# Kernel optimization log

Hardware: AMD Instinct MI355X
Metric: run time of the kernel (lower is better)

The kernel has to match this reference:

```python
import jax, jax.numpy as jnp
import numpy as np
from jax import lax

C_IN, C_OUT, K, N_BASE, HIDDEN = 256, 256, 3, 8, 128
ATT_TAU = 1.0


def setup_inputs() -> dict:
    key = jax.random.key(0)
    ks = jax.random.split(key, 6)
    B, H, W = 64, 64, 64
    x = jax.random.normal(ks[0], (B, C_IN, H, W), dtype=jnp.float32)
    # attention MLP params (torch Linear convention: W is [out, in])
    w1 = jax.random.normal(ks[1], (HIDDEN, C_IN), dtype=jnp.float32) * (1.0 / np.sqrt(C_IN))
    b1 = jnp.zeros((HIDDEN,), dtype=jnp.float32)
    w2 = jax.random.normal(ks[2], (C_OUT * N_BASE, HIDDEN), dtype=jnp.float32) * (1.0 / np.sqrt(HIDDEN))
    b2 = jnp.zeros((C_OUT * N_BASE,), dtype=jnp.float32)
    # base filters: kaiming-normal over flat [n_base, c_in*k*k]
    fan_in = C_IN * K * K
    base_filters = jax.random.normal(ks[3], (N_BASE, fan_in), dtype=jnp.float32) * np.sqrt(2.0 / fan_in)
    return {"x": x, "w1": w1, "b1": b1, "w2": w2, "b2": b2, "base_filters": base_filters}


def reference(x, w1, b1, w2, b2, base_filters):
    B = x.shape[0]
    # global average pool -> [B, c_in]
    pooled = x.mean(axis=(2, 3))
    # attention MLP -> per-sample mixing weights [B, c_out, n_base]
    h = jax.nn.relu(pooled @ w1.T + b1)
    mix = (h @ w2.T + b2).reshape(B, C_OUT, N_BASE)
    mix = jax.nn.softmax(mix / ATT_TAU, axis=2)
    # base conv: [B, c_in, H, W] -> [B, n_base, H, W], SAME padding (k//2)
    filt = base_filters.reshape(N_BASE, C_IN, K, K)
    pad = K // 2
    y = lax.conv_general_dilated(
        x, filt, window_strides=(1, 1), padding=[(pad, pad), (pad, pad)],
        dimension_numbers=("NCHW", "OIHW", "NCHW"))
    # per-sample 1x1 mixing conv == batched matmul over channels
    out = jnp.einsum("bon,bnhw->bohw", mix, y)
    return out
```

## Files before the change

### kernel.cpp

```cpp
#include <hip/hip_runtime.h>
#include <math.h>

#define CIN 256
#define COUT 256
#define NB 8
#define HID 128
#define HW 4096
#define BATCH 64

__global__ __launch_bounds__(256) void repack_filters(
    const float* __restrict__ bf, float* __restrict__ fT) {
  int i = blockIdx.x * 256 + threadIdx.x;
  if (i < 8 * 2304) {
    int n = i / 2304;
    int cd = i % 2304;
    fT[cd * 8 + n] = bf[i];
  }
}

__global__ __launch_bounds__(256) void conv_pool_kernel(
    const float* __restrict__ x, const float* __restrict__ fT,
    float* __restrict__ ypart, float* __restrict__ poolpart) {
  __shared__ float xs[8 * 34 * 68];
  const int t = threadIdx.x;
  const int bid = blockIdx.x;
  const int b = bid >> 2;
  const int chhalf = (bid >> 1) & 1;
  const int rchunk = bid & 1;
  const int row0 = rchunk * 32;
  const int c0 = chhalf * 128;

  for (int i = t; i < 8 * 34 * 68; i += 256) xs[i] = 0.0f;
  __syncthreads();

  const int ch = t >> 5;
  const int part = t & 31;
  const int r = t >> 3;
  const int cg = t & 7;

  float acc[8][8];
#pragma unroll
  for (int n = 0; n < 8; ++n)
#pragma unroll
    for (int j = 0; j < 8; ++j) acc[n][j] = 0.0f;

  for (int chunk = 0; chunk < 16; ++chunk) {
    const int cbase = c0 + chunk * 8;
    float psum = 0.0f;
    const float* xsrc = x + ((size_t)(b * CIN + cbase + ch) * HW);
#pragma unroll
    for (int i = 0; i < 17; ++i) {
      int s = part + i * 32;
      int row = s >> 4;
      int seg = s & 15;
      int grow = row0 + row - 1;
      if (grow >= 0 && grow < 64) {
        const float4 v = *(const float4*)(xsrc + grow * 64 + seg * 4);
        float* dst = &xs[(ch * 34 + row) * 68 + 1 + seg * 4];
        dst[0] = v.x; dst[1] = v.y; dst[2] = v.z; dst[3] = v.w;
        if (row >= 1 && row < 33) psum += (v.x + v.y) + (v.z + v.w);
      }
    }
#pragma unroll
    for (int off = 16; off > 0; off >>= 1)
      psum += __shfl_down(psum, off, 32);
    if (part == 0)
      poolpart[(b * 2 + rchunk) * 256 + cbase + ch] = psum;
    __syncthreads();

#pragma unroll
    for (int cc = 0; cc < 8; ++cc) {
      const float* fb = fT + (size_t)(cbase + cc) * 72;
      const float* xrow = &xs[(cc * 34 + r) * 68 + cg * 8];
#pragma unroll
      for (int dy = 0; dy < 3; ++dy) {
        const float* xr = xrow + dy * 68;
        float w[10];
        float4 a0 = *(const float4*)(xr);
        float4 a1 = *(const float4*)(xr + 4);
        float2 a2 = *(const float2*)(xr + 8);
        w[0] = a0.x; w[1] = a0.y; w[2] = a0.z; w[3] = a0.w;
        w[4] = a1.x; w[5] = a1.y; w[6] = a1.z; w[7] = a1.w;
        w[8] = a2.x; w[9] = a2.y;
#pragma unroll
        for (int dx = 0; dx < 3; ++dx) {
#pragma unroll
          for (int n = 0; n < 8; ++n) {
            const float fv = fb[(dy * 3 + dx) * 8 + n];
#pragma unroll
            for (int j = 0; j < 8; ++j)
              acc[n][j] = fmaf(w[j + dx], fv, acc[n][j]);
          }
        }
      }
    }
    __syncthreads();
  }

#pragma unroll
  for (int n = 0; n < 8; ++n) {
    float* yp = ypart +
        ((size_t)(((b * 2 + chhalf) * 8 + n) * 64 + row0 + r) * 64 + cg * 8);
    float4 v0 = {acc[n][0], acc[n][1], acc[n][2], acc[n][3]};
    float4 v1 = {acc[n][4], acc[n][5], acc[n][6], acc[n][7]};
    *(float4*)(yp) = v0;
    *(float4*)(yp + 4) = v1;
  }
}

__global__ __launch_bounds__(256) void mlp_kernel(
    const float* __restrict__ poolpart, const float* __restrict__ w1,
    const float* __restrict__ b1, const float* __restrict__ w2,
    const float* __restrict__ b2, float* __restrict__ mix) {
  __shared__ float pool_s[256];
  __shared__ float h_s[128];
  const int t = threadIdx.x;
  const int b = blockIdx.x;
  pool_s[t] = (poolpart[(b * 2 + 0) * 256 + t] +
               poolpart[(b * 2 + 1) * 256 + t]) * (1.0f / 4096.0f);
  __syncthreads();
  if (t < 128) {
    float a = b1[t];
    const float* wr = w1 + t * 256;
    for (int c = 0; c < 256; c += 4) {
      float4 wv = *(const float4*)(wr + c);
      a = fmaf(pool_s[c], wv.x, a);
      a = fmaf(pool_s[c + 1], wv.y, a);
      a = fmaf(pool_s[c + 2], wv.z, a);
      a = fmaf(pool_s[c + 3], wv.w, a);
    }
    h_s[t] = fmaxf(a, 0.0f);
  }
  __syncthreads();
  float m[8];
#pragma unroll
  for (int n = 0; n < 8; ++n) {
    float a = b2[t * 8 + n];
    const float* wr = w2 + (size_t)(t * 8 + n) * 128;
    for (int j = 0; j < 128; j += 4) {
      float4 wv = *(const float4*)(wr + j);
      a = fmaf(h_s[j], wv.x, a);
      a = fmaf(h_s[j + 1], wv.y, a);
      a = fmaf(h_s[j + 2], wv.z, a);
      a = fmaf(h_s[j + 3], wv.w, a);
    }
    m[n] = a;
  }
  float mx = m[0];
#pragma unroll
  for (int n = 1; n < 8; ++n) mx = fmaxf(mx, m[n]);
  float s = 0.0f;
#pragma unroll
  for (int n = 0; n < 8; ++n) {
    m[n] = __expf(m[n] - mx);
    s += m[n];
  }
  float inv = 1.0f / s;
#pragma unroll
  for (int n = 0; n < 8; ++n) mix[(size_t)(b * 256 + t) * 8 + n] = m[n] * inv;
}

__global__ __launch_bounds__(256) void mix_conv_kernel(
    const float* __restrict__ ypart, const float* __restrict__ mix,
    float* __restrict__ out) {
  __shared__ float ys[8 * 1024];
  __shared__ float mix_s[2048];
  const int t = threadIdx.x;
  const int b = blockIdx.x >> 2;
  const int tile = blockIdx.x & 3;
  const int p0 = tile * 1024;

  const float* y0 = ypart + (size_t)(b * 2 + 0) * 8 * HW + p0;
  const float* y1 = ypart + (size_t)(b * 2 + 1) * 8 * HW + p0;
  for (int i = t; i < 2048; i += 256) {
    int n = i >> 8;
    int pv = i & 255;
    float4 a = *(const float4*)(y0 + n * HW + pv * 4);
    float4 c = *(const float4*)(y1 + n * HW + pv * 4);
    float4 r = {a.x + c.x, a.y + c.y, a.z + c.z, a.w + c.w};
    *(float4*)&ys[n * 1024 + pv * 4] = r;
  }
  {
    const float4* ms = (const float4*)(mix + (size_t)b * 2048);
    float4* md = (float4*)mix_s;
    for (int i = t; i < 512; i += 256) md[i] = ms[i];
  }
  __syncthreads();

  float4 y4[8];
#pragma unroll
  for (int n = 0; n < 8; ++n) y4[n] = *(const float4*)&ys[n * 1024 + t * 4];

  float* op = out + (size_t)b * COUT * HW + p0 + t * 4;
  for (int o = 0; o < 256; ++o) {
    float4 ma = *(const float4*)&mix_s[o * 8];
    float4 mb = *(const float4*)&mix_s[o * 8 + 4];
    float4 r;
    r.x = ma.x * y4[0].x; r.y = ma.x * y4[0].y;
    r.z = ma.x * y4[0].z; r.w = ma.x * y4[0].w;
    r.x = fmaf(ma.y, y4[1].x, r.x); r.y = fmaf(ma.y, y4[1].y, r.y);
    r.z = fmaf(ma.y, y4[1].z, r.z); r.w = fmaf(ma.y, y4[1].w, r.w);
    r.x = fmaf(ma.z, y4[2].x, r.x); r.y = fmaf(ma.z, y4[2].y, r.y);
    r.z = fmaf(ma.z, y4[2].z, r.z); r.w = fmaf(ma.z, y4[2].w, r.w);
    r.x = fmaf(ma.w, y4[3].x, r.x); r.y = fmaf(ma.w, y4[3].y, r.y);
    r.z = fmaf(ma.w, y4[3].z, r.z); r.w = fmaf(ma.w, y4[3].w, r.w);
    r.x = fmaf(mb.x, y4[4].x, r.x); r.y = fmaf(mb.x, y4[4].y, r.y);
    r.z = fmaf(mb.x, y4[4].z, r.z); r.w = fmaf(mb.x, y4[4].w, r.w);
    r.x = fmaf(mb.y, y4[5].x, r.x); r.y = fmaf(mb.y, y4[5].y, r.y);
    r.z = fmaf(mb.y, y4[5].z, r.z); r.w = fmaf(mb.y, y4[5].w, r.w);
    r.x = fmaf(mb.z, y4[6].x, r.x); r.y = fmaf(mb.z, y4[6].y, r.y);
    r.z = fmaf(mb.z, y4[6].z, r.z); r.w = fmaf(mb.z, y4[6].w, r.w);
    r.x = fmaf(mb.w, y4[7].x, r.x); r.y = fmaf(mb.w, y4[7].y, r.y);
    r.z = fmaf(mb.w, y4[7].z, r.z); r.w = fmaf(mb.w, y4[7].w, r.w);
    *(float4*)(op + (size_t)o * HW) = r;
  }
}

extern "C" void kernel_launch(void* const* d_in, const int* in_sizes, int n_in,
                              void* d_out, int out_size, void* d_ws,
                              size_t ws_size, hipStream_t stream) {
  const float* x  = (const float*)d_in[0];
  const float* w1 = (const float*)d_in[1];
  const float* b1 = (const float*)d_in[2];
  const float* w2 = (const float*)d_in[3];
  const float* b2 = (const float*)d_in[4];
  const float* bf = (const float*)d_in[5];
  float* out = (float*)d_out;

  char* ws = (char*)d_ws;
  float* ypart    = (float*)(ws);
  float* poolpart = (float*)(ws + 16777216);
  float* mixw     = (float*)(ws + 16777216 + 131072);
  float* fT       = (float*)(ws + 16777216 + 131072 + 2097152);

  repack_filters<<<72, 256, 0, stream>>>(bf, fT);
  conv_pool_kernel<<<256, 256, 0, stream>>>(x, fT, ypart, poolpart);
  mlp_kernel<<<64, 256, 0, stream>>>(poolpart, w1, b1, w2, b2, mixw);
  mix_conv_kernel<<<256, 256, 0, stream>>>(ypart, mixw, out);
}
```

Measured before the change: 692.3 us.

## Split conv into smaller tiles and channel quarters for more blocks

New measurement: 581.1 us. 16.1% less time.

```diff
diff --git a/kernel.cpp b/kernel.cpp
--- a/kernel.cpp
+++ b/kernel.cpp
@@ -7,6 +7,9 @@
 #define HID 128
 #define HW 4096
 #define BATCH 64
+
+#define TROWS 18
+#define XSTR 68
 
 __global__ __launch_bounds__(256) void repack_filters(
     const float* __restrict__ bf, float* __restrict__ fT) {
@@ -18,77 +21,76 @@
   }
 }
 
-__global__ __launch_bounds__(256) void conv_pool_kernel(
+__global__ __launch_bounds__(256, 4) void conv_pool_kernel(
     const float* __restrict__ x, const float* __restrict__ fT,
     float* __restrict__ ypart, float* __restrict__ poolpart) {
-  __shared__ float xs[8 * 34 * 68];
+  __shared__ float xs[8 * TROWS * XSTR];
   const int t = threadIdx.x;
   const int bid = blockIdx.x;
-  const int b = bid >> 2;
-  const int chhalf = (bid >> 1) & 1;
-  const int rchunk = bid & 1;
-  const int row0 = rchunk * 32;
-  const int c0 = chhalf * 128;
-
-  for (int i = t; i < 8 * 34 * 68; i += 256) xs[i] = 0.0f;
+  const int b = bid >> 4;
+  const int g = (bid >> 2) & 3;
+  const int rc = bid & 3;
+  const int row0 = rc * 16;
+  const int c0 = g * 64;
+
+  for (int i = t; i < 8 * TROWS * XSTR; i += 256) xs[i] = 0.0f;
   __syncthreads();
 
   const int ch = t >> 5;
   const int part = t & 31;
-  const int r = t >> 3;
-  const int cg = t & 7;
-
-  float acc[8][8];
+  const int r = t >> 4;
+  const int cg = t & 15;
+
+  float acc[8][4];
 #pragma unroll
   for (int n = 0; n < 8; ++n)
 #pragma unroll
-    for (int j = 0; j < 8; ++j) acc[n][j] = 0.0f;
-
-  for (int chunk = 0; chunk < 16; ++chunk) {
+    for (int j = 0; j < 4; ++j) acc[n][j] = 0.0f;
+
+#pragma unroll 1
+  for (int chunk = 0; chunk < 8; ++chunk) {
     const int cbase = c0 + chunk * 8;
     float psum = 0.0f;
     const float* xsrc = x + ((size_t)(b * CIN + cbase + ch) * HW);
 #pragma unroll
-    for (int i = 0; i < 17; ++i) {
+    for (int i = 0; i < 9; ++i) {
       int s = part + i * 32;
       int row = s >> 4;
       int seg = s & 15;
       int grow = row0 + row - 1;
       if (grow >= 0 && grow < 64) {
         const float4 v = *(const float4*)(xsrc + grow * 64 + seg * 4);
-        float* dst = &xs[(ch * 34 + row) * 68 + 1 + seg * 4];
+        float* dst = &xs[(ch * TROWS + row) * XSTR + 1 + seg * 4];
         dst[0] = v.x; dst[1] = v.y; dst[2] = v.z; dst[3] = v.w;
-        if (row >= 1 && row < 33) psum += (v.x + v.y) + (v.z + v.w);
+        if (row >= 1 && row <= 16) psum += (v.x + v.y) + (v.z + v.w);
       }
     }
 #pragma unroll
     for (int off = 16; off > 0; off >>= 1)
       psum += __shfl_down(psum, off, 32);
     if (part == 0)
-      poolpart[(b * 2 + rchunk) * 256 + cbase + ch] = psum;
+      poolpart[(b * 4 + rc) * 256 + cbase + ch] = psum;
     __syncthreads();
 
 #pragma unroll
     for (int cc = 0; cc < 8; ++cc) {
       const float* fb = fT + (size_t)(cbase + cc) * 72;
-      const float* xrow = &xs[(cc * 34 + r) * 68 + cg * 8];
+      const float* xrow = &xs[(cc * TROWS + r) * XSTR + cg * 4];
 #pragma unroll
       for (int dy = 0; dy < 3; ++dy) {
-        const float* xr = xrow + dy * 68;
-        float w[10];
+        const float* xr = xrow + dy * XSTR;
         float4 a0 = *(const float4*)(xr);
-        float4 a1 = *(const float4*)(xr + 4);
-        float2 a2 = *(const float2*)(xr + 8);
+        float2 a1 = *(const float2*)(xr + 4);
+        float w[6];
         w[0] = a0.x; w[1] = a0.y; w[2] = a0.z; w[3] = a0.w;
-        w[4] = a1.x; w[5] = a1.y; w[6] = a1.z; w[7] = a1.w;
-        w[8] = a2.x; w[9] = a2.y;
+        w[4] = a1.x; w[5] = a1.y;
 #pragma unroll
         for (int dx = 0; dx < 3; ++dx) {
 #pragma unroll
           for (int n = 0; n < 8; ++n) {
             const float fv = fb[(dy * 3 + dx) * 8 + n];
 #pragma unroll
-            for (int j = 0; j < 8; ++j)
+            for (int j = 0; j < 4; ++j)
               acc[n][j] = fmaf(w[j + dx], fv, acc[n][j]);
           }
         }
@@ -100,11 +102,9 @@
 #pragma unroll
   for (int n = 0; n < 8; ++n) {
     float* yp = ypart +
-        ((size_t)(((b * 2 + chhalf) * 8 + n) * 64 + row0 + r) * 64 + cg * 8);
+        ((size_t)(((b * 4 + g) * 8 + n) * 64 + row0 + r) * 64 + cg * 4);
     float4 v0 = {acc[n][0], acc[n][1], acc[n][2], acc[n][3]};
-    float4 v1 = {acc[n][4], acc[n][5], acc[n][6], acc[n][7]};
     *(float4*)(yp) = v0;
-    *(float4*)(yp + 4) = v1;
   }
 }
 
@@ -116,8 +116,10 @@
   __shared__ float h_s[128];
   const int t = threadIdx.x;
   const int b = blockIdx.x;
-  pool_s[t] = (poolpart[(b * 2 + 0) * 256 + t] +
-               poolpart[(b * 2 + 1) * 256 + t]) * (1.0f / 4096.0f);
+  pool_s[t] = (poolpart[(b * 4 + 0) * 256 + t] +
+               poolpart[(b * 4 + 1) * 256 + t] +
+               poolpart[(b * 4 + 2) * 256 + t] +
+               poolpart[(b * 4 + 3) * 256 + t]) * (1.0f / 4096.0f);
   __syncthreads();
   if (t < 128) {
     float a = b1[t];
@@ -170,15 +172,18 @@
   const int tile = blockIdx.x & 3;
   const int p0 = tile * 1024;
 
-  const float* y0 = ypart + (size_t)(b * 2 + 0) * 8 * HW + p0;
-  const float* y1 = ypart + (size_t)(b * 2 + 1) * 8 * HW + p0;
+  const float* yb = ypart + (size_t)b * 4 * 8 * HW + p0;
   for (int i = t; i < 2048; i += 256) {
     int n = i >> 8;
     int pv = i & 255;
-    float4 a = *(const float4*)(y0 + n * HW + pv * 4);
-    float4 c = *(const float4*)(y1 + n * HW + pv * 4);
-    float4 r = {a.x + c.x, a.y + c.y, a.z + c.z, a.w + c.w};
-    *(float4*)&ys[n * 1024 + pv * 4] = r;
+    const float* y0 = yb + n * HW + pv * 4;
+    float4 a = *(const float4*)(y0);
+    float4 c = *(const float4*)(y0 + 8 * HW);
+    float4 d = *(const float4*)(y0 + 16 * HW);
+    float4 e = *(const float4*)(y0 + 24 * HW);
+    float4 rr = {a.x + c.x + d.x + e.x, a.y + c.y + d.y + e.y,
+                 a.z + c.z + d.z + e.z, a.w + c.w + d.w + e.w};
+    *(float4*)&ys[n * 1024 + pv * 4] = rr;
   }
   {
     const float4* ms = (const float4*)(mix + (size_t)b * 2048);
@@ -229,12 +234,12 @@
 
   char* ws = (char*)d_ws;
   float* ypart    = (float*)(ws);
-  float* poolpart = (float*)(ws + 16777216);
-  float* mixw     = (float*)(ws + 16777216 + 131072);
-  float* fT       = (float*)(ws + 16777216 + 131072 + 2097152);
+  float* poolpart = (float*)(ws + 33554432);
+  float* mixw     = (float*)(ws + 33554432 + 262144);
+  float* fT       = (float*)(ws + 33554432 + 262144 + 2097152);
 
   repack_filters<<<72, 256, 0, stream>>>(bf, fT);
-  conv_pool_kernel<<<256, 256, 0, stream>>>(x, fT, ypart, poolpart);
+  conv_pool_kernel<<<1024, 256, 0, stream>>>(x, fT, ypart, poolpart);
   mlp_kernel<<<64, 256, 0, stream>>>(poolpart, w1, b1, w2, b2, mixw);
   mix_conv_kernel<<<256, 256, 0, stream>>>(ypart, mixw, out);
 }
```
